# Performance work log

Hardware: AMD Instinct MI355X
Metric: run time of the kernel (lower is better)

## Reference

```python
import jax, jax.numpy as jnp
import numpy as np

H = 768   # hidden_size
E = 9     # num_entity_types
R = 10    # num_relation_types
B, S, N = 8, 4096, 64
P = N * (N - 1) // 2  # 2016 ordered pairs i<j


def setup_inputs() -> dict:
    key = jax.random.key(0)
    ks = jax.random.split(key, 10)
    sd = 0.02
    return {
        "sequence_output": jax.random.normal(ks[0], (B, S, H), jnp.float32),
        "attention_mask": jnp.ones((B, S), jnp.int32),
        "entity_spans": jnp.sort(jax.random.randint(ks[1], (B, N, 2), 0, S), axis=-1),
        # entity_classifier: Linear(H, H//2) -> ReLU -> Linear(H//2, E)
        "w1": jax.random.normal(ks[2], (H, H // 2), jnp.float32) * sd,
        "b1": jnp.zeros((H // 2,), jnp.float32),
        "w2": jax.random.normal(ks[3], (H // 2, E), jnp.float32) * sd,
        "b2": jnp.zeros((E,), jnp.float32),
        # relation_classifier: Linear(2H, H) -> ReLU -> Linear(H, R)
        "rw1": jax.random.normal(ks[4], (2 * H, H), jnp.float32) * sd,
        "rb1": jnp.zeros((H,), jnp.float32),
        "rw2": jax.random.normal(ks[5], (H, R), jnp.float32) * sd,
        "rb2": jnp.zeros((R,), jnp.float32),
    }


def reference(sequence_output, attention_mask, entity_spans,
              w1, b1, w2, b2, rw1, rb1, rw2, rb2):
    # entity classifier over all tokens (dropout is identity in eval)
    h = jax.nn.relu(jnp.einsum('bsh,hf->bsf', sequence_output, w1) + b1)
    entity_logits = jnp.einsum('bsf,fe->bse', h, w2) + b2  # [B,S,E]

    # span mean-pooling via a [B,N,S] membership mask (segment-mean)
    pos = jnp.arange(S)
    start = entity_spans[..., 0:1]  # [B,N,1]
    end = entity_spans[..., 1:2]    # [B,N,1]
    mask = ((pos >= start) & (pos < end)).astype(sequence_output.dtype)  # [B,N,S]
    counts = jnp.clip(mask.sum(-1, keepdims=True), 1.0)  # avoid /0 for empty spans
    entity_reprs = jnp.einsum('bns,bsh->bnh', mask, sequence_output) / counts  # [B,N,H]
    pooled_logits = jnp.einsum('bns,bse->bne', mask, entity_logits) / counts   # [B,N,E]
    entity_types = jnp.argmax(pooled_logits, axis=-1)  # [B,N]

    # all i<j pairs, batched relation classifier (replaces per-pair Python loop)
    ii, jj = np.triu_indices(N, k=1)  # static index sets, len P
    pair = jnp.concatenate([entity_reprs[:, ii], entity_reprs[:, jj]], axis=-1)  # [B,P,2H]
    rh = jax.nn.relu(jnp.einsum('bpk,kh->bph', pair, rw1) + rb1)
    relation_logits = jnp.einsum('bph,hr->bpr', rh, rw2) + rb2  # [B,P,R]
    relation_types = jnp.argmax(relation_logits, axis=-1)  # [B,P]

    return entity_logits, relation_logits, entity_reprs, entity_types, relation_types
```

## Files before the change

### kernel.cpp

```cpp
#include <hip/hip_runtime.h>
#include <hip/hip_bf16.h>

#define Hh 768
#define Ff 384
#define Ee 9
#define Rr 10
#define Bb 8
#define Ss 4096
#define Nn_ENT 64
#define Pp 2016
#define CH 16
#define NC 256

typedef short bf16x8 __attribute__((ext_vector_type(8)));
typedef float f32x4 __attribute__((ext_vector_type(4)));

__device__ __forceinline__ void async_copy16(void* lds, const void* g) {
  auto* l = (__attribute__((address_space(3))) unsigned int*)(lds);
  auto* p = (const __attribute__((address_space(1))) unsigned int*)(g);
  __builtin_amdgcn_global_load_lds(p, l, 16, 0, 0);
}

__global__ __launch_bounds__(256) void transpose_w1(const float* __restrict__ w1,
                                                    unsigned short* __restrict__ wt) {
  __shared__ unsigned short tile[64][65];
  const int bk = blockIdx.x * 64;
  const int bc = blockIdx.y * 64;
  const int c = threadIdx.x & 63, kq = threadIdx.x >> 6;
#pragma unroll
  for (int i = 0; i < 16; ++i) {
    int k = kq * 16 + i;
    float v = w1[(size_t)(bk + k) * Ff + bc + c];
    tile[c][k] = __bfloat16_as_ushort(__float2bfloat16(v));
  }
  __syncthreads();
  const int k2 = threadIdx.x & 63, cq = threadIdx.x >> 6;
#pragma unroll
  for (int i = 0; i < 16; ++i) {
    int c2 = cq * 16 + i;
    wt[(size_t)(bc + c2) * Hh + bk + k2] = tile[c2][k2];
  }
}

__global__ __launch_bounds__(512, 4) void gemm1_fused(const float* __restrict__ A,
                                                      const unsigned short* __restrict__ Wt,
                                                      const float* __restrict__ b1,
                                                      const float* __restrict__ w2,
                                                      const float* __restrict__ b2,
                                                      float* __restrict__ elog,
                                                      float* __restrict__ Pc) {
  __shared__ float As[64 * 64];
  __shared__ unsigned short Bs[384 * 64];
  __shared__ float w2s[Ff * Ee];
  __shared__ float b1s[Ff];
  __shared__ float b2s[Ee];
  float* red = (float*)&Bs[0];

  const int t = threadIdx.x;
  const int wid = t >> 6, lane = t & 63;
  const int wm = wid >> 2, wn = wid & 3;
  const int fr = lane & 15, fq = lane >> 4;
  const int row0 = blockIdx.x * 64;
  const int bb = row0 >> 12;
  const int c0 = (row0 & (Ss - 1)) >> 4;

  for (int i = t; i < Ff * Ee; i += 512) w2s[i] = w2[i];
  for (int i = t; i < Ff; i += 512) b1s[i] = b1[i];
  if (t < Ee) b2s[t] = b2[t];

  const int brow0 = (lane >> 3);
  const int bgr = lane & 7;

  f32x4 acc[2][6] = {};
  const int sB = (fr & 7);

#pragma unroll 1
  for (int ks = 0; ks < Hh / 64; ++ks) {
    const int k0 = ks * 64;
#pragma unroll
    for (int i = 0; i < 2; ++i) {
      const int rl = (wid * 2 + i) * 4 + (lane >> 4);
      const int g = (lane & 15) ^ (rl & 15);
      async_copy16(&As[(wid * 2 + i) * 256],
                   A + (size_t)(row0 + rl) * Hh + k0 + g * 4);
    }
#pragma unroll
    for (int j = 0; j < 6; ++j) {
      const int e = wid * 6 + j;
      const int rl = e * 8 + brow0;
      const int g = bgr ^ (rl & 7);
      async_copy16(&Bs[e * 512],
                   Wt + (size_t)rl * Hh + k0 + g * 8);
    }
    __syncthreads();

#pragma unroll
    for (int kk = 0; kk < 2; ++kk) {
      bf16x8 af[2], bfr[6];
#pragma unroll
      for (int m = 0; m < 2; ++m) {
        const int R = wm * 32 + m * 16 + fr;
        const int G0 = 2 * (kk * 4 + fq);
        const float* rowp = &As[R * 64];
        float4 v0 = *(const float4*)(rowp + ((G0 ^ fr) * 4));
        float4 v1 = *(const float4*)(rowp + (((G0 + 1) ^ fr) * 4));
        union { bf16x8 v; __hip_bfloat162 h2[4]; } u;
        u.h2[0] = __float22bfloat162_rn(float2{v0.x, v0.y});
        u.h2[1] = __float22bfloat162_rn(float2{v0.z, v0.w});
        u.h2[2] = __float22bfloat162_rn(float2{v1.x, v1.y});
        u.h2[3] = __float22bfloat162_rn(float2{v1.z, v1.w});
        af[m] = u.v;
      }
      const int gB = ((kk * 4 + fq) ^ sB) * 8;
#pragma unroll
      for (int n = 0; n < 6; ++n)
        bfr[n] = *(const bf16x8*)&Bs[(wn * 96 + n * 16 + fr) * 64 + gB];
#pragma unroll
      for (int m = 0; m < 2; ++m)
#pragma unroll
        for (int n = 0; n < 6; ++n)
          acc[m][n] = __builtin_amdgcn_mfma_f32_16x16x32_bf16(af[m], bfr[n], acc[m][n], 0, 0, 0);
    }

    if (t < 256) {
      const int cc = t >> 6, kq = lane & 15, rh = lane >> 4;
      float4 s = {0.f, 0.f, 0.f, 0.f};
#pragma unroll
      for (int q = 0; q < 4; ++q) {
        const int row = cc * 16 + rh * 4 + q;
        const int slot = kq ^ (rh * 4 + q);
        float4 v = *(const float4*)&As[row * 64 + slot * 4];
        s.x += v.x; s.y += v.y; s.z += v.z; s.w += v.w;
      }
      s.x += __shfl_xor(s.x, 16); s.y += __shfl_xor(s.y, 16);
      s.z += __shfl_xor(s.z, 16); s.w += __shfl_xor(s.w, 16);
      s.x += __shfl_xor(s.x, 32); s.y += __shfl_xor(s.y, 32);
      s.z += __shfl_xor(s.z, 32); s.w += __shfl_xor(s.w, 32);
      if (rh == 0)
        *(float4*)&Pc[((size_t)(bb * NC + c0 + cc)) * Hh + k0 + kq * 4] = s;
    }
    __syncthreads();
  }

#pragma unroll
  for (int m = 0; m < 2; ++m) {
#pragma unroll
    for (int j = 0; j < 4; ++j) {
      float p[Ee];
#pragma unroll
      for (int e = 0; e < Ee; ++e) p[e] = 0.f;
#pragma unroll
      for (int n = 0; n < 6; ++n) {
        const int col = wn * 96 + n * 16 + fr;
        const float hv = fmaxf(acc[m][n][j] + b1s[col], 0.f);
        const float* wrow = &w2s[col * Ee];
#pragma unroll
        for (int e = 0; e < Ee; ++e) p[e] = fmaf(hv, wrow[e], p[e]);
      }
#pragma unroll
      for (int mask = 1; mask <= 8; mask <<= 1)
#pragma unroll
        for (int e = 0; e < Ee; ++e) p[e] += __shfl_xor(p[e], mask);
      if (fr < Ee) {
        const int row = wm * 32 + m * 16 + fq * 4 + j;
        red[(wn * 64 + row) * Ee + fr] = p[fr];
      }
    }
  }
  __syncthreads();
  for (int idx = t; idx < 64 * Ee; idx += 512) {
    const int row = idx / Ee, e = idx - row * Ee;
    float v = red[(0 * 64 + row) * Ee + e] + red[(1 * 64 + row) * Ee + e]
            + red[(2 * 64 + row) * Ee + e] + red[(3 * 64 + row) * Ee + e] + b2s[e];
    elog[(size_t)(row0 + row) * Ee + e] = v;
  }
}

__global__ __launch_bounds__(256) void gemm_uv_splitk(const float* __restrict__ A,
                                                      const float* __restrict__ rw1,
                                                      float* __restrict__ part) {
  const int uv = blockIdx.z & 1, ks = blockIdx.z >> 1;
  const float* Wp = rw1 + (size_t)uv * Hh * Hh + (size_t)ks * 192 * Hh;
  __shared__ float Ast[16][68];
  __shared__ float Wst[16][68];
  const int t = threadIdx.x;
  const int row0 = blockIdx.x * 64, col0 = blockIdx.y * 64;
  const int tm = (t & 15) * 4, tn = (t >> 4) * 4;
  const int lr = t >> 2, lk = (t & 3) * 4;
  const int wk = t >> 4, wc = (t & 15) * 4;
  float acc[4][4] = {};
  const float* Arow = A + (size_t)(row0 + lr) * Hh + ks * 192 + lk;
  for (int k0 = 0; k0 < 192; k0 += 16) {
    float4 av = *(const float4*)(Arow + k0);
    Ast[lk + 0][lr] = av.x; Ast[lk + 1][lr] = av.y;
    Ast[lk + 2][lr] = av.z; Ast[lk + 3][lr] = av.w;
    *(float4*)&Wst[wk][wc] = *(const float4*)(Wp + (size_t)(k0 + wk) * Hh + col0 + wc);
    __syncthreads();
#pragma unroll
    for (int kk = 0; kk < 16; ++kk) {
      const float4 a = *(const float4*)&Ast[kk][tm];
      const float4 b = *(const float4*)&Wst[kk][tn];
      acc[0][0] = fmaf(a.x, b.x, acc[0][0]); acc[0][1] = fmaf(a.x, b.y, acc[0][1]);
      acc[0][2] = fmaf(a.x, b.z, acc[0][2]); acc[0][3] = fmaf(a.x, b.w, acc[0][3]);
      acc[1][0] = fmaf(a.y, b.x, acc[1][0]); acc[1][1] = fmaf(a.y, b.y, acc[1][1]);
      acc[1][2] = fmaf(a.y, b.z, acc[1][2]); acc[1][3] = fmaf(a.y, b.w, acc[1][3]);
      acc[2][0] = fmaf(a.z, b.x, acc[2][0]); acc[2][1] = fmaf(a.z, b.y, acc[2][1]);
      acc[2][2] = fmaf(a.z, b.z, acc[2][2]); acc[2][3] = fmaf(a.z, b.w, acc[2][3]);
      acc[3][0] = fmaf(a.w, b.x, acc[3][0]); acc[3][1] = fmaf(a.w, b.y, acc[3][1]);
      acc[3][2] = fmaf(a.w, b.z, acc[3][2]); acc[3][3] = fmaf(a.w, b.w, acc[3][3]);
    }
    __syncthreads();
  }
  float* out = part + ((size_t)ks * 2 + uv) * (512 * Hh);
#pragma unroll
  for (int i = 0; i < 4; ++i) {
    float4 o; o.x = acc[i][0]; o.y = acc[i][1]; o.z = acc[i][2]; o.w = acc[i][3];
    *(float4*)(out + (size_t)(row0 + tm + i) * Hh + col0 + tn) = o;
  }
}

__global__ __launch_bounds__(256) void uv_reduce(const float* __restrict__ part,
                                                 float* __restrict__ uv) {
  const int i = blockIdx.x * 256 + threadIdx.x;
  const float4* p = (const float4*)part;
  float4 a = p[i], b = p[i + 196608], c = p[i + 2 * 196608], d = p[i + 3 * 196608];
  float4 o;
  o.x = (a.x + b.x) + (c.x + d.x);
  o.y = (a.y + b.y) + (c.y + d.y);
  o.z = (a.z + b.z) + (c.z + d.z);
  o.w = (a.w + b.w) + (c.w + d.w);
  ((float4*)uv)[i] = o;
}

__global__ __launch_bounds__(256) void chunk_scan(float* __restrict__ Pc) {
  __shared__ float tile[NC][64];
  const int b = blockIdx.y;
  const int h0 = blockIdx.x * 64;
  float* base = Pc + (size_t)b * NC * Hh + h0;
  const int l = threadIdx.x & 63, g = threadIdx.x >> 6;
#pragma unroll 4
  for (int c = g * 64; c < g * 64 + 64; ++c)
    tile[c][l] = base[(size_t)c * Hh + l];
  __syncthreads();
  float run = 0.f;
#pragma unroll 4
  for (int c = g * 64; c < g * 64 + 64; ++c) {
    run += tile[c][l];
    tile[c][l] = run;
  }
  __syncthreads();
  float off = 0.f;
#pragma unroll
  for (int gg = 0; gg < 3; ++gg)
    if (gg < g) off += tile[gg * 64 + 63][l];
  __syncthreads();
  if (g > 0) {
#pragma unroll 4
    for (int c = g * 64; c < g * 64 + 64; ++c)
      tile[c][l] += off;
  }
  __syncthreads();
#pragma unroll 4
  for (int c = g * 64; c < g * 64 + 64; ++c)
    base[(size_t)c * Hh + l] = tile[c][l];
}

__global__ __launch_bounds__(192) void entity_reprs_k(const float* __restrict__ seq,
                                                      const float* __restrict__ Pc,
                                                      const int* __restrict__ spans,
                                                      float* __restrict__ reprs) {
  const int bn = blockIdx.x;
  const int b = bn >> 6;
  const int start = spans[bn * 2], end = spans[bn * 2 + 1];
  const int cnt = max(end - start, 1);
  const float inv = 1.0f / (float)cnt;
  const int cs = (start + CH - 1) >> 4, ce = end >> 4;
  const float* seqb = seq + (size_t)b * Ss * Hh;
  const float4* Pcb = (const float4*)(Pc + (size_t)b * NC * Hh);
  const int t = threadIdx.x;
  float4 acc = {0.f, 0.f, 0.f, 0.f};
  if (cs <= ce) {
    if (cs < ce) {
      float4 hi = Pcb[(size_t)(ce - 1) * 192 + t];
      acc.x += hi.x; acc.y += hi.y; acc.z += hi.z; acc.w += hi.w;
      if (cs > 0) {
        float4 lo = Pcb[(size_t)(cs - 1) * 192 + t];
        acc.x -= lo.x; acc.y -= lo.y; acc.z -= lo.z; acc.w -= lo.w;
      }
    }
    for (int s = start; s < cs * CH; ++s) {
      float4 v = ((const float4*)(seqb + (size_t)s * Hh))[t];
      acc.x += v.x; acc.y += v.y; acc.z += v.z; acc.w += v.w;
    }
    for (int s = ce * CH; s < end; ++s) {
      float4 v = ((const float4*)(seqb + (size_t)s * Hh))[t];
      acc.x += v.x; acc.y += v.y; acc.z += v.z; acc.w += v.w;
    }
  } else {
    for (int s = start; s < end; ++s) {
      float4 v = ((const float4*)(seqb + (size_t)s * Hh))[t];
      acc.x += v.x; acc.y += v.y; acc.z += v.z; acc.w += v.w;
    }
  }
  float4 o; o.x = acc.x * inv; o.y = acc.y * inv; o.z = acc.z * inv; o.w = acc.w * inv;
  ((float4*)(reprs + (size_t)bn * Hh))[t] = o;
}

__global__ __launch_bounds__(256) void pooled_argmax(const float* __restrict__ elog,
                                                     const int* __restrict__ spans,
                                                     float* __restrict__ etypes) {
  __shared__ float red[4][Ee];
  const int bn = blockIdx.x;
  const int b = bn >> 6;
  const int start = spans[bn * 2], end = spans[bn * 2 + 1];
  const int t = threadIdx.x, lane = t & 63, w = t >> 6;
  float acc[Ee];
#pragma unroll
  for (int e = 0; e < Ee; ++e) acc[e] = 0.f;
  const float* p = elog + (size_t)b * Ss * Ee;
  for (int s = start + t; s < end; s += 256) {
    const float* q = p + (size_t)s * Ee;
#pragma unroll
    for (int e = 0; e < Ee; ++e) acc[e] += q[e];
  }
#pragma unroll
  for (int off = 32; off; off >>= 1)
#pragma unroll
    for (int e = 0; e < Ee; ++e) acc[e] += __shfl_down(acc[e], off);
  if (lane == 0) {
#pragma unroll
    for (int e = 0; e < Ee; ++e) red[w][e] = acc[e];
  }
  __syncthreads();
  if (t == 0) {
    int best = 0; float bv = -1e30f;
#pragma unroll
    for (int e = 0; e < Ee; ++e) {
      float v = red[0][e] + red[1][e] + red[2][e] + red[3][e];
      if (v > bv) { bv = v; best = e; }
    }
    etypes[bn] = (float)best;
  }
}

__global__ __launch_bounds__(256) void relations_k(const float* __restrict__ UV,
                                                   const float* __restrict__ rb1,
                                                   const float* __restrict__ rw2,
                                                   const float* __restrict__ rb2,
                                                   float* __restrict__ rlogits,
                                                   float* __restrict__ rtypes) {
  __shared__ float w2l[Hh * 11];
  __shared__ float b1l[Hh];
  const int t = threadIdx.x;
  for (int i = t; i < Hh * Rr; i += 256) {
    const int k = i / Rr, r = i - k * Rr;
    w2l[k * 11 + r] = rw2[i];
  }
  for (int i = t; i < Hh; i += 256) b1l[i] = rb1[i];
  __syncthreads();

  const int lane = t & 63;
  const int pbase = blockIdx.x * 16 + (t >> 6) * 4;
#pragma unroll 1
  for (int pi = 0; pi < 4; ++pi) {
    const int p = pbase + pi;
    const int b = p / Pp, pp = p % Pp;
    int i = 0, off = 0;
    while (off + (Nn_ENT - 1 - i) <= pp) { off += Nn_ENT - 1 - i; ++i; }
    const int j = i + 1 + (pp - off);
    const float* u = UV + ((size_t)b * Nn_ENT + i) * Hh;
    const float* v = UV + (size_t)512 * Hh + ((size_t)b * Nn_ENT + j) * Hh;
    float acc[Rr];
#pragma unroll
    for (int r = 0; r < Rr; ++r) acc[r] = 0.f;
    for (int k = lane; k < Hh; k += 64) {
      float x = fmaxf(u[k] + v[k] + b1l[k], 0.f);
      const float* w = &w2l[k * 11];
#pragma unroll
      for (int r = 0; r < Rr; ++r) acc[r] = fmaf(x, w[r], acc[r]);
    }
#pragma unroll
    for (int off2 = 32; off2; off2 >>= 1)
#pragma unroll
      for (int r = 0; r < Rr; ++r) acc[r] += __shfl_down(acc[r], off2);
    if (lane == 0) {
      int best = 0; float bv = acc[0] + rb2[0];
      rlogits[(size_t)p * Rr + 0] = bv;
#pragma unroll
      for (int r = 1; r < Rr; ++r) {
        float val = acc[r] + rb2[r];
        rlogits[(size_t)p * Rr + r] = val;
        if (val > bv) { bv = val; best = r; }
      }
      rtypes[p] = (float)best;
    }
  }
}

extern "C" void kernel_launch(void* const* d_in, const int* in_sizes, int n_in,
                              void* d_out, int out_size, void* d_ws, size_t ws_size,
                              hipStream_t stream) {
  const float* seq   = (const float*)d_in[0];
  const int*   spans = (const int*)d_in[2];
  const float* w1    = (const float*)d_in[3];
  const float* b1    = (const float*)d_in[4];
  const float* w2    = (const float*)d_in[5];
  const float* b2    = (const float*)d_in[6];
  const float* rw1   = (const float*)d_in[7];
  const float* rb1   = (const float*)d_in[8];
  const float* rw2   = (const float*)d_in[9];
  const float* rb2   = (const float*)d_in[10];

  float* out_elog = (float*)d_out;
  float* out_rlog = out_elog + 294912;
  float* out_repr = out_rlog + 161280;
  float* out_etyp = out_repr + 393216;
  float* out_rtyp = out_etyp + 512;

  float*          ws_pc  = (float*)d_ws;
  float*          ws_uv  = (float*)((char*)d_ws + 6291456);
  unsigned short* ws_wt  = (unsigned short*)((char*)d_ws + 9437184);
  float*          ws_uvp = (float*)((char*)d_ws + 10027008);

  transpose_w1<<<dim3(12, 6), 256, 0, stream>>>(w1, ws_wt);
  gemm1_fused<<<512, 512, 0, stream>>>(seq, ws_wt, b1, w2, b2, out_elog, ws_pc);
  chunk_scan<<<dim3(Hh / 64, Bb), 256, 0, stream>>>(ws_pc);
  entity_reprs_k<<<512, 192, 0, stream>>>(seq, ws_pc, spans, out_repr);
  gemm_uv_splitk<<<dim3(8, 12, 8), 256, 0, stream>>>(out_repr, rw1, ws_uvp);
  uv_reduce<<<768, 256, 0, stream>>>(ws_uvp, ws_uv);
  pooled_argmax<<<512, 256, 0, stream>>>(out_elog, spans, out_etyp);
  relations_k<<<1008, 256, 0, stream>>>(ws_uv, rb1, rw2, rb2, out_rlog, out_rtyp);
}
```

Baseline: 139.3 us.

## Double-buffer gemm1 LDS tiles to overlap async global loads with MFMA

Splits the A and W tiles of the fused entity-classifier GEMM into two LDS buffers and prefetches the next K-slice with async global-to-LDS copies while the current slice is computed. Explicit vmcnt waits and barriers replace the per-iteration __syncthreads pair, so load latency is hidden behind MFMA work. This doubles the LDS footprint, and the launch bound drops from 4 to 2 blocks per CU, which lowers occupancy.

```diff
diff --git a/kernel.cpp b/kernel.cpp
--- a/kernel.cpp
+++ b/kernel.cpp
@@ -42,19 +42,21 @@
   }
 }
 
-__global__ __launch_bounds__(512, 4) void gemm1_fused(const float* __restrict__ A,
+__global__ __launch_bounds__(512, 2) void gemm1_fused(const float* __restrict__ A,
                                                       const unsigned short* __restrict__ Wt,
                                                       const float* __restrict__ b1,
                                                       const float* __restrict__ w2,
                                                       const float* __restrict__ b2,
                                                       float* __restrict__ elog,
                                                       float* __restrict__ Pc) {
-  __shared__ float As[64 * 64];
-  __shared__ unsigned short Bs[384 * 64];
+  __shared__ float As0[64 * 64];
+  __shared__ unsigned short Bs0[384 * 64];
+  __shared__ float As1[64 * 64];
+  __shared__ unsigned short Bs1[384 * 64];
   __shared__ float w2s[Ff * Ee];
   __shared__ float b1s[Ff];
   __shared__ float b2s[Ee];
-  float* red = (float*)&Bs[0];
+  float* red = (float*)&As0[0];
 
   const int t = threadIdx.x;
   const int wid = t >> 6, lane = t & 63;
@@ -74,73 +76,108 @@
   f32x4 acc[2][6] = {};
   const int sB = (fr & 7);
 
+#define STAGE(ASB, BSB, ks) do {                                             \
+    const int k0s = (ks) * 64;                                               \
+    _Pragma("unroll")                                                        \
+    for (int i = 0; i < 2; ++i) {                                            \
+      const int rl = (wid * 2 + i) * 4 + (lane >> 4);                        \
+      const int g = (lane & 15) ^ (rl & 15);                                 \
+      async_copy16(&ASB[(wid * 2 + i) * 256],                                \
+                   A + (size_t)(row0 + rl) * Hh + k0s + g * 4);              \
+    }                                                                        \
+    _Pragma("unroll")                                                        \
+    for (int j = 0; j < 6; ++j) {                                            \
+      const int e = wid * 6 + j;                                             \
+      const int rl = e * 8 + brow0;                                          \
+      const int g = bgr ^ (rl & 7);                                          \
+      async_copy16(&BSB[e * 512],                                            \
+                   Wt + (size_t)rl * Hh + k0s + g * 8);                      \
+    }                                                                        \
+  } while (0)
+
+#define COMPUTE(ASB, BSB, ks) do {                                           \
+    const int k0s = (ks) * 64;                                               \
+    _Pragma("unroll")                                                        \
+    for (int kk = 0; kk < 2; ++kk) {                                         \
+      bf16x8 af[2], bfr[6];                                                  \
+      _Pragma("unroll")                                                      \
+      for (int m = 0; m < 2; ++m) {                                          \
+        const int R = wm * 32 + m * 16 + fr;                                 \
+        const int G0 = 2 * (kk * 4 + fq);                                    \
+        const float* rowp = &ASB[R * 64];                                    \
+        float4 v0 = *(const float4*)(rowp + ((G0 ^ fr) * 4));                \
+        float4 v1 = *(const float4*)(rowp + (((G0 + 1) ^ fr) * 4));          \
+        union { bf16x8 v; __hip_bfloat162 h2[4]; } u;                        \
+        u.h2[0] = __float22bfloat162_rn(float2{v0.x, v0.y});                 \
+        u.h2[1] = __float22bfloat162_rn(float2{v0.z, v0.w});                 \
+        u.h2[2] = __float22bfloat162_rn(float2{v1.x, v1.y});                 \
+        u.h2[3] = __float22bfloat162_rn(float2{v1.z, v1.w});                 \
+        af[m] = u.v;                                                         \
+      }                                                                      \
+      const int gB = ((kk * 4 + fq) ^ sB) * 8;                               \
+      _Pragma("unroll")                                                      \
+      for (int n = 0; n < 6; ++n)                                            \
+        bfr[n] = *(const bf16x8*)&BSB[(wn * 96 + n * 16 + fr) * 64 + gB];    \
+      _Pragma("unroll")                                                      \
+      for (int m = 0; m < 2; ++m)                                            \
+        _Pragma("unroll")                                                    \
+        for (int n = 0; n < 6; ++n)                                          \
+          acc[m][n] = __builtin_amdgcn_mfma_f32_16x16x32_bf16(af[m], bfr[n], acc[m][n], 0, 0, 0); \
+    }                                                                        \
+    if (t < 256) {                                                           \
+      const int cc = t >> 6, kq = lane & 15, rh = lane >> 4;                 \
+      float4 s = {0.f, 0.f, 0.f, 0.f};                                       \
+      _Pragma("unroll")                                                      \
+      for (int q = 0; q < 4; ++q) {                                          \
+        const int row = cc * 16 + rh * 4 + q;                                \
+        const int slot = kq ^ (rh * 4 + q);                                  \
+        float4 v = *(const float4*)&ASB[row * 64 + slot * 4];                \
+        s.x += v.x; s.y += v.y; s.z += v.z; s.w += v.w;                      \
+      }                                                                      \
+      s.x += __shfl_xor(s.x, 16); s.y += __shfl_xor(s.y, 16);                \
+      s.z += __shfl_xor(s.z, 16); s.w += __shfl_xor(s.w, 16);                \
+      s.x += __shfl_xor(s.x, 32); s.y += __shfl_xor(s.y, 32);                \
+      s.z += __shfl_xor(s.z, 32); s.w += __shfl_xor(s.w, 32);                \
+      if (rh == 0)                                                           \
+        *(float4*)&Pc[((size_t)(bb * NC + c0 + cc)) * Hh + k0s + kq * 4] = s;\
+    }                                                                        \
+  } while (0)
+
+#define WAIT_STAGE8() do {                                                   \
+    asm volatile("s_waitcnt vmcnt(8)" ::: "memory");                         \
+    __builtin_amdgcn_s_barrier();                                            \
+    __builtin_amdgcn_sched_barrier(0);                                       \
+  } while (0)
+#define WAIT_STAGE0() do {                                                   \
+    asm volatile("s_waitcnt vmcnt(0)" ::: "memory");                         \
+    __builtin_amdgcn_s_barrier();                                            \
+    __builtin_amdgcn_sched_barrier(0);                                       \
+  } while (0)
+#define END_READS() do {                                                     \
+    __builtin_amdgcn_sched_barrier(0);                                       \
+    __builtin_amdgcn_s_barrier();                                            \
+    __builtin_amdgcn_sched_barrier(0);                                       \
+  } while (0)
+
+  STAGE(As0, Bs0, 0);
+  STAGE(As1, Bs1, 1);
+
 #pragma unroll 1
-  for (int ks = 0; ks < Hh / 64; ++ks) {
-    const int k0 = ks * 64;
-#pragma unroll
-    for (int i = 0; i < 2; ++i) {
-      const int rl = (wid * 2 + i) * 4 + (lane >> 4);
-      const int g = (lane & 15) ^ (rl & 15);
-      async_copy16(&As[(wid * 2 + i) * 256],
-                   A + (size_t)(row0 + rl) * Hh + k0 + g * 4);
-    }
-#pragma unroll
-    for (int j = 0; j < 6; ++j) {
-      const int e = wid * 6 + j;
-      const int rl = e * 8 + brow0;
-      const int g = bgr ^ (rl & 7);
-      async_copy16(&Bs[e * 512],
-                   Wt + (size_t)rl * Hh + k0 + g * 8);
-    }
-    __syncthreads();
-
-#pragma unroll
-    for (int kk = 0; kk < 2; ++kk) {
-      bf16x8 af[2], bfr[6];
-#pragma unroll
-      for (int m = 0; m < 2; ++m) {
-        const int R = wm * 32 + m * 16 + fr;
-        const int G0 = 2 * (kk * 4 + fq);
-        const float* rowp = &As[R * 64];
-        float4 v0 = *(const float4*)(rowp + ((G0 ^ fr) * 4));
-        float4 v1 = *(const float4*)(rowp + (((G0 + 1) ^ fr) * 4));
-        union { bf16x8 v; __hip_bfloat162 h2[4]; } u;
-        u.h2[0] = __float22bfloat162_rn(float2{v0.x, v0.y});
-        u.h2[1] = __float22bfloat162_rn(float2{v0.z, v0.w});
-        u.h2[2] = __float22bfloat162_rn(float2{v1.x, v1.y});
-        u.h2[3] = __float22bfloat162_rn(float2{v1.z, v1.w});
-        af[m] = u.v;
-      }
-      const int gB = ((kk * 4 + fq) ^ sB) * 8;
-#pragma unroll
-      for (int n = 0; n < 6; ++n)
-        bfr[n] = *(const bf16x8*)&Bs[(wn * 96 + n * 16 + fr) * 64 + gB];
-#pragma unroll
-      for (int m = 0; m < 2; ++m)
-#pragma unroll
-        for (int n = 0; n < 6; ++n)
-          acc[m][n] = __builtin_amdgcn_mfma_f32_16x16x32_bf16(af[m], bfr[n], acc[m][n], 0, 0, 0);
-    }
-
-    if (t < 256) {
-      const int cc = t >> 6, kq = lane & 15, rh = lane >> 4;
-      float4 s = {0.f, 0.f, 0.f, 0.f};
-#pragma unroll
-      for (int q = 0; q < 4; ++q) {
-        const int row = cc * 16 + rh * 4 + q;
-        const int slot = kq ^ (rh * 4 + q);
-        float4 v = *(const float4*)&As[row * 64 + slot * 4];
-        s.x += v.x; s.y += v.y; s.z += v.z; s.w += v.w;
-      }
-      s.x += __shfl_xor(s.x, 16); s.y += __shfl_xor(s.y, 16);
-      s.z += __shfl_xor(s.z, 16); s.w += __shfl_xor(s.w, 16);
-      s.x += __shfl_xor(s.x, 32); s.y += __shfl_xor(s.y, 32);
-      s.z += __shfl_xor(s.z, 32); s.w += __shfl_xor(s.w, 32);
-      if (rh == 0)
-        *(float4*)&Pc[((size_t)(bb * NC + c0 + cc)) * Hh + k0 + kq * 4] = s;
-    }
-    __syncthreads();
-  }
+  for (int ks = 0; ks < Hh / 64; ks += 2) {
+    WAIT_STAGE8();
+    COMPUTE(As0, Bs0, ks);
+    END_READS();
+    if (ks + 2 < Hh / 64) STAGE(As0, Bs0, ks + 2);
+    if (ks + 2 < Hh / 64) { WAIT_STAGE8(); } else { WAIT_STAGE0(); }
+    COMPUTE(As1, Bs1, ks + 1);
+    END_READS();
+    if (ks + 3 < Hh / 64) STAGE(As1, Bs1, ks + 3);
+  }
+#undef STAGE
+#undef COMPUTE
+#undef WAIT_STAGE8
+#undef WAIT_STAGE0
+#undef END_READS
 
 #pragma unroll
   for (int m = 0; m < 2; ++m) {
```

New measurement: 157.2 us. 12.9% more time.
